# Performance work log

Measured on AMD Instinct MI355X. Metric: run time of the kernel, lower is better.

The kernel has to match this reference:

```python
import jax, jax.numpy as jnp
import numpy as np

NUM_EMBEDDINGS = 512
EMBEDDING_DIM = 128
COMMITMENT_COST = 0.6
MID_HR = 100.0
HR_RANGE = 70.0


def setup_inputs() -> dict:
    key = jax.random.key(0)
    k1, k2 = jax.random.split(key)
    inputs = jax.random.normal(k1, (64, 2048, EMBEDDING_DIM), dtype=jnp.float32)
    # torch init: uniform(-1/K, 1/K)
    emb_weight = jax.random.uniform(
        k2, (NUM_EMBEDDINGS, EMBEDDING_DIM), dtype=jnp.float32,
        minval=-1.0 / NUM_EMBEDDINGS, maxval=1.0 / NUM_EMBEDDINGS)
    scaling = jnp.ones((NUM_EMBEDDINGS,), dtype=jnp.float32)
    return {"inputs": inputs, "emb_weight": emb_weight, "scaling": scaling}


def reference(inputs, emb_weight, scaling):
    B, T, D = inputs.shape
    K = emb_weight.shape[0]
    flat = inputs.reshape(-1, D)  # [N, D]
    # squared L2 distances to all codes: [N, K]
    distances = (
        jnp.sum(flat * flat, axis=1, keepdims=True)
        + jnp.sum(emb_weight * emb_weight, axis=1)
        - 2.0 * flat @ emb_weight.T
    )
    hr_values = jnp.linspace(40.0, 180.0, K, dtype=jnp.float32)
    hr_weights = 1.0 + scaling * ((hr_values - MID_HR) / HR_RANGE)  # [K]
    encoding_indices = jnp.argmin(distances * hr_weights[None, :], axis=1)  # [N]
    # one-hot @ codebook == direct gather
    quantized = emb_weight[encoding_indices].reshape(inputs.shape)
    e_latent_loss = jnp.mean((jax.lax.stop_gradient(quantized) - inputs) ** 2)
    q_latent_loss = jnp.mean((quantized - jax.lax.stop_gradient(inputs)) ** 2)
    loss = q_latent_loss + COMMITMENT_COST * e_latent_loss
    # straight-through estimator
    quantized_st = inputs + jax.lax.stop_gradient(quantized - inputs)
    return quantized_st, loss, encoding_indices.reshape(B, T)
```

## Files before the change

kernel.cpp:

```cpp
#include <hip/hip_runtime.h>

#define NCODES 512
#define DIM 128
#define NROWS (64*2048)
#define QN (NROWS*DIM)
#define BLK_ROWS 512
#define NBLOCKS (NROWS/BLK_ROWS)
#define NWAVES 16

typedef __attribute__((ext_vector_type(8))) short short8;
typedef __attribute__((ext_vector_type(4))) float f32x4;

__device__ __forceinline__ unsigned short f2bf(float f) {
  unsigned u = __builtin_bit_cast(unsigned, f);
  u += 0x7FFFu + ((u >> 16) & 1u);
  return (unsigned short)(u >> 16);
}

#define GLOAD_LDS16(gp, lp) __builtin_amdgcn_global_load_lds( \
    (__attribute__((address_space(1))) void*)(gp), \
    (__attribute__((address_space(3))) void*)(lp), 16, 0, 0)

__global__ void vq_prep(const float* __restrict__ emb, const float* __restrict__ scaling,
                        unsigned short* __restrict__ emb_bf,
                        float* __restrict__ wv, float* __restrict__ wse,
                        float* __restrict__ wrcp) {
  int k = blockIdx.x;
  int l = threadIdx.x;
  float2 v = ((const float2*)(emb + k * DIM))[l];
  float ss = v.x * v.x + v.y * v.y;
#pragma unroll
  for (int m = 1; m < 64; m <<= 1) ss += __shfl_xor(ss, m);
  unsigned pack = (unsigned)f2bf(v.x) | ((unsigned)f2bf(v.y) << 16);
  ((unsigned*)emb_bf)[k * 64 + l] = pack;
  if (l == 0) {
    float hr = 40.0f + (float)k * (140.0f / 511.0f);
    float wt = 1.0f + scaling[k] * ((hr - 100.0f) * (1.0f / 70.0f));
    wv[k] = wt;
    wse[k] = wt * ss;
    wrcp[k] = 1.0f / wt;
  }
}

struct SmemT {
  unsigned short frag[NCODES * DIM];
  float w[NCODES];
  float wse[NCODES];
  float wrcp[NCODES];
  float lossp[NWAVES];
};

__global__ __launch_bounds__(1024, 4) void vq_main(
    const float* __restrict__ x,
    const float* __restrict__ emb32,
    const unsigned short* __restrict__ emb_bf,
    const float* __restrict__ wv,
    const float* __restrict__ wse,
    const float* __restrict__ wrcp,
    float* __restrict__ out_q,
    float* __restrict__ out_idx,
    float* __restrict__ out_loss) {
  __shared__ SmemT sm;
  const int tid = threadIdx.x;
  const int wave = tid >> 6, lane = tid & 63;
  const int g = lane >> 4, lr = lane & 15;
  const long rowbase = (long)blockIdx.x * BLK_ROWS + wave * 32;

  float4 xv[2][4][2];
#pragma unroll
  for (int rg = 0; rg < 2; rg++) {
    const float* xr = x + (rowbase + rg * 16 + lr) * DIM + g * 8;
#pragma unroll
    for (int c = 0; c < 4; c++) {
      xv[rg][c][0] = *(const float4*)(xr + c * 32);
      xv[rg][c][1] = *(const float4*)(xr + c * 32 + 4);
    }
  }

  {
    const uint4* src = (const uint4*)emb_bf;
#pragma unroll
    for (int i = 0; i < 8; i++) {
      int winst = wave * 8 + i;
      int d = winst * 64 + lane;
      int t = d >> 8, c = (d >> 6) & 3, gg = (d >> 4) & 3, rr = d & 15;
      int s = (t * 16 + rr) * 16 + c * 4 + gg;
      GLOAD_LDS16(src + s, (char*)sm.frag + winst * 1024);
    }
    if (tid < NCODES) {
      sm.w[tid] = wv[tid];
      sm.wse[tid] = wse[tid];
      sm.wrcp[tid] = wrcp[tid];
    }
  }

  short8 a[2][4];
  float sr[2][4];
  {
    float srow[2];
#pragma unroll
    for (int rg = 0; rg < 2; rg++) {
      float ss = 0.f;
#pragma unroll
      for (int c = 0; c < 4; c++) {
        float4 v0 = xv[rg][c][0];
        float4 v1 = xv[rg][c][1];
        ss += v0.x * v0.x + v0.y * v0.y + v0.z * v0.z + v0.w * v0.w;
        ss += v1.x * v1.x + v1.y * v1.y + v1.z * v1.z + v1.w * v1.w;
        short8 av;
        av[0] = (short)f2bf(v0.x); av[1] = (short)f2bf(v0.y);
        av[2] = (short)f2bf(v0.z); av[3] = (short)f2bf(v0.w);
        av[4] = (short)f2bf(v1.x); av[5] = (short)f2bf(v1.y);
        av[6] = (short)f2bf(v1.z); av[7] = (short)f2bf(v1.w);
        a[rg][c] = av;
      }
      ss += __shfl_xor(ss, 16);
      ss += __shfl_xor(ss, 32);
      srow[rg] = ss;
    }
#pragma unroll
    for (int rg = 0; rg < 2; rg++)
#pragma unroll
      for (int r = 0; r < 4; r++)
        sr[rg][r] = __shfl(srow[rg], g * 4 + r);
  }
  __syncthreads();

  unsigned pmin[2][4];
#pragma unroll
  for (int rg = 0; rg < 2; rg++)
#pragma unroll
    for (int r = 0; r < 4; r++) pmin[rg][r] = 0xFFFFFFFFu;

  const short8* __restrict__ bbase = (const short8*)sm.frag + lane;
#pragma unroll 2
  for (int t = 0; t < 32; t++) {
    const unsigned code = t * 16 + lr;
    const float wt = sm.w[code];
    const float bb = sm.wse[code];
    const float m2w = -2.0f * wt;
    f32x4 acc0 = {0.f, 0.f, 0.f, 0.f};
    f32x4 acc1 = {0.f, 0.f, 0.f, 0.f};
#pragma unroll
    for (int c = 0; c < 4; c++) {
      short8 bf = bbase[(t * 4 + c) * 64];
      acc0 = __builtin_amdgcn_mfma_f32_16x16x32_bf16(a[0][c], bf, acc0, 0, 0, 0);
      acc1 = __builtin_amdgcn_mfma_f32_16x16x32_bf16(a[1][c], bf, acc1, 0, 0, 0);
    }
#pragma unroll
    for (int r = 0; r < 4; r++) {
      float v0 = fmaf(m2w, acc0[r], fmaf(wt, sr[0][r], bb));
      float v1 = fmaf(m2w, acc1[r], fmaf(wt, sr[1][r], bb));
      unsigned u0 = (__builtin_bit_cast(unsigned, v0) & 0xFFFFFE00u) | code;
      unsigned u1 = (__builtin_bit_cast(unsigned, v1) & 0xFFFFFE00u) | code;
      pmin[0][r] = min(pmin[0][r], u0);
      pmin[1][r] = min(pmin[1][r], u1);
    }
  }

#pragma unroll
  for (int m = 1; m <= 8; m <<= 1) {
#pragma unroll
    for (int rg = 0; rg < 2; rg++)
#pragma unroll
      for (int r = 0; r < 4; r++) {
        unsigned o = (unsigned)__shfl_xor((int)pmin[rg][r], m);
        pmin[rg][r] = min(pmin[rg][r], o);
      }
  }

  const uint4* __restrict__ esrc = (const uint4*)emb32;
  uint4* __restrict__ outu = (uint4*)out_q + rowbase * 32;
  const int col = lane & 31;
  const int hi = lane >> 5;
  int scode[16];
#pragma unroll
  for (int it = 0; it < 16; it++) {
    const int row0 = 2 * it;
    const int rg = row0 >> 4;
    const int gn = (row0 >> 2) & 3;
    const int r0 = row0 & 3;
    int c0 = __shfl((int)pmin[rg][r0], gn * 16);
    int c1 = __shfl((int)pmin[rg][r0 + 1], gn * 16);
    scode[it] = (hi ? c1 : c0) & 511;
  }

  uint4 vbuf[8];
#pragma unroll
  for (int j = 0; j < 8; j++)
    vbuf[j] = esrc[scode[j] * 32 + col];

  {
    float l0 = 0.f;
#pragma unroll
    for (int rg = 0; rg < 2; rg++)
#pragma unroll
      for (int r = 0; r < 4; r++) {
        unsigned wn = pmin[rg][r];
        int ci = (int)(wn & 511u);
        float dist = __builtin_bit_cast(float, wn & 0xFFFFFE00u);
        l0 = fmaf(dist, sm.wrcp[ci], l0);
        if (lr == 0) out_idx[rowbase + rg * 16 + g * 4 + r] = (float)ci;
      }
    l0 += __shfl_xor(l0, 16);
    l0 += __shfl_xor(l0, 32);
    if (lane == 0) sm.lossp[wave] = l0;
  }

#pragma unroll
  for (int j = 0; j < 8; j++)
    outu[j * 64 + lane] = vbuf[j];
#pragma unroll
  for (int j = 0; j < 8; j++)
    vbuf[j] = esrc[scode[8 + j] * 32 + col];
#pragma unroll
  for (int j = 0; j < 8; j++)
    outu[(8 + j) * 64 + lane] = vbuf[j];

  __syncthreads();
  if (wave == 0 && lane < NWAVES) {
    float s = sm.lossp[lane];
#pragma unroll
    for (int m = 1; m < NWAVES; m <<= 1) s += __shfl_xor(s, m);
    if (lane == 0) atomicAdd(out_loss, s * (1.6f / (float)QN));
  }
}

extern "C" void kernel_launch(void* const* d_in, const int* in_sizes, int n_in,
                              void* d_out, int out_size, void* d_ws, size_t ws_size,
                              hipStream_t stream) {
  const float* x = (const float*)d_in[0];
  const float* emb = (const float*)d_in[1];
  const float* scaling = (const float*)d_in[2];

  float* out_q = (float*)d_out;
  float* out_loss = out_q + QN;
  float* out_idx = out_q + QN + 1;

  unsigned short* emb_bf = (unsigned short*)d_ws;
  float* wv = (float*)((char*)d_ws + NCODES * DIM * 2);
  float* wse = wv + NCODES;
  float* wrcp = wse + NCODES;

  hipMemsetAsync(out_loss, 0, sizeof(float), stream);
  vq_prep<<<NCODES, 64, 0, stream>>>(emb, scaling, emb_bf, wv, wse, wrcp);
  vq_main<<<NBLOCKS, 1024, 0, stream>>>(x, emb, emb_bf, wv, wse, wrcp,
                                        out_q, out_idx, out_loss);
}
```

Measured before the change: 49.27 us.

## Switch distance matmul from bf16 to fp8 MFMA with scaled codebook and smaller blocks

Converts inputs and codebook to fp8 (e4m3, codebook pre-scaled by 512 and laid out in fragment order during prep) and uses the 16x16x32 fp8 MFMA instead of bf16. This halves the shared-memory codebook footprint and the LDS read traffic. The block size is halved to 512 threads / 256 rows to raise occupancy. The risk is argmin mismatches from the much lower fp8 precision of both operands, especially near-tie distances, which could change the returned indices versus the reference.

```diff
diff --git a/kernel.cpp b/kernel.cpp
--- a/kernel.cpp
+++ b/kernel.cpp
@@ -4,25 +4,18 @@
 #define DIM 128
 #define NROWS (64*2048)
 #define QN (NROWS*DIM)
-#define BLK_ROWS 512
+#define BLK_ROWS 256
 #define NBLOCKS (NROWS/BLK_ROWS)
-#define NWAVES 16
-
-typedef __attribute__((ext_vector_type(8))) short short8;
+#define NWAVES 8
+
 typedef __attribute__((ext_vector_type(4))) float f32x4;
-
-__device__ __forceinline__ unsigned short f2bf(float f) {
-  unsigned u = __builtin_bit_cast(unsigned, f);
-  u += 0x7FFFu + ((u >> 16) & 1u);
-  return (unsigned short)(u >> 16);
-}
 
 #define GLOAD_LDS16(gp, lp) __builtin_amdgcn_global_load_lds( \
     (__attribute__((address_space(1))) void*)(gp), \
     (__attribute__((address_space(3))) void*)(lp), 16, 0, 0)
 
 __global__ void vq_prep(const float* __restrict__ emb, const float* __restrict__ scaling,
-                        unsigned short* __restrict__ emb_bf,
+                        unsigned char* __restrict__ e8frag,
                         float* __restrict__ wv, float* __restrict__ wse,
                         float* __restrict__ wrcp) {
   int k = blockIdx.x;
@@ -31,8 +24,11 @@
   float ss = v.x * v.x + v.y * v.y;
 #pragma unroll
   for (int m = 1; m < 64; m <<= 1) ss += __shfl_xor(ss, m);
-  unsigned pack = (unsigned)f2bf(v.x) | ((unsigned)f2bf(v.y) << 16);
-  ((unsigned*)emb_bf)[k * 64 + l] = pack;
+  int p = __builtin_amdgcn_cvt_pk_fp8_f32(v.x * 512.0f, v.y * 512.0f, 0, false);
+  int t = k >> 4, col = k & 15;
+  int c = l >> 4, g = (l >> 2) & 3, jp = l & 3;
+  *(unsigned short*)(e8frag + (((t * 4 + c) * 64 + g * 16 + col) << 3) + 2 * jp) =
+      (unsigned short)(p & 0xFFFF);
   if (l == 0) {
     float hr = 40.0f + (float)k * (140.0f / 511.0f);
     float wt = 1.0f + scaling[k] * ((hr - 100.0f) * (1.0f / 70.0f));
@@ -43,17 +39,17 @@
 }
 
 struct SmemT {
-  unsigned short frag[NCODES * DIM];
+  unsigned char frag[NCODES * DIM];
   float w[NCODES];
   float wse[NCODES];
   float wrcp[NCODES];
   float lossp[NWAVES];
 };
 
-__global__ __launch_bounds__(1024, 4) void vq_main(
+__global__ __launch_bounds__(512, 4) void vq_main(
     const float* __restrict__ x,
     const float* __restrict__ emb32,
-    const unsigned short* __restrict__ emb_bf,
+    const unsigned char* __restrict__ e8frag,
     const float* __restrict__ wv,
     const float* __restrict__ wse,
     const float* __restrict__ wrcp,
@@ -78,23 +74,16 @@
   }
 
   {
-    const uint4* src = (const uint4*)emb_bf;
 #pragma unroll
     for (int i = 0; i < 8; i++) {
-      int winst = wave * 8 + i;
-      int d = winst * 64 + lane;
-      int t = d >> 8, c = (d >> 6) & 3, gg = (d >> 4) & 3, rr = d & 15;
-      int s = (t * 16 + rr) * 16 + c * 4 + gg;
-      GLOAD_LDS16(src + s, (char*)sm.frag + winst * 1024);
-    }
-    if (tid < NCODES) {
-      sm.w[tid] = wv[tid];
-      sm.wse[tid] = wse[tid];
-      sm.wrcp[tid] = wrcp[tid];
-    }
-  }
-
-  short8 a[2][4];
+      int slot = i * 512 + tid;
+      GLOAD_LDS16(e8frag + slot * 16, sm.frag + slot * 16);
+    }
+    sm.w[tid] = wv[tid]; sm.wse[tid] = wse[tid]; sm.wrcp[tid] = wrcp[tid];
+    int t2 = tid + 512 - 512; (void)t2;
+  }
+
+  long a[2][4];
   float sr[2][4];
   {
     float srow[2];
@@ -107,12 +96,12 @@
         float4 v1 = xv[rg][c][1];
         ss += v0.x * v0.x + v0.y * v0.y + v0.z * v0.z + v0.w * v0.w;
         ss += v1.x * v1.x + v1.y * v1.y + v1.z * v1.z + v1.w * v1.w;
-        short8 av;
-        av[0] = (short)f2bf(v0.x); av[1] = (short)f2bf(v0.y);
-        av[2] = (short)f2bf(v0.z); av[3] = (short)f2bf(v0.w);
-        av[4] = (short)f2bf(v1.x); av[5] = (short)f2bf(v1.y);
-        av[6] = (short)f2bf(v1.z); av[7] = (short)f2bf(v1.w);
-        a[rg][c] = av;
+        int lo = __builtin_amdgcn_cvt_pk_fp8_f32(v0.x, v0.y, 0, false);
+        lo = __builtin_amdgcn_cvt_pk_fp8_f32(v0.z, v0.w, lo, true);
+        int hi = __builtin_amdgcn_cvt_pk_fp8_f32(v1.x, v1.y, 0, false);
+        hi = __builtin_amdgcn_cvt_pk_fp8_f32(v1.z, v1.w, hi, true);
+        a[rg][c] = (long)(((unsigned long long)(unsigned)hi << 32) |
+                          (unsigned long long)(unsigned)lo);
       }
       ss += __shfl_xor(ss, 16);
       ss += __shfl_xor(ss, 32);
@@ -132,20 +121,20 @@
 #pragma unroll
     for (int r = 0; r < 4; r++) pmin[rg][r] = 0xFFFFFFFFu;
 
-  const short8* __restrict__ bbase = (const short8*)sm.frag + lane;
+  const long* __restrict__ bbase = (const long*)sm.frag + lane;
 #pragma unroll 2
   for (int t = 0; t < 32; t++) {
     const unsigned code = t * 16 + lr;
     const float wt = sm.w[code];
     const float bb = sm.wse[code];
-    const float m2w = -2.0f * wt;
+    const float m2w = -2.0f * wt * (1.0f / 512.0f);
     f32x4 acc0 = {0.f, 0.f, 0.f, 0.f};
     f32x4 acc1 = {0.f, 0.f, 0.f, 0.f};
 #pragma unroll
     for (int c = 0; c < 4; c++) {
-      short8 bf = bbase[(t * 4 + c) * 64];
-      acc0 = __builtin_amdgcn_mfma_f32_16x16x32_bf16(a[0][c], bf, acc0, 0, 0, 0);
-      acc1 = __builtin_amdgcn_mfma_f32_16x16x32_bf16(a[1][c], bf, acc1, 0, 0, 0);
+      long bf = bbase[(t * 4 + c) * 64];
+      acc0 = __builtin_amdgcn_mfma_f32_16x16x32_fp8_fp8(a[0][c], bf, acc0, 0, 0, 0);
+      acc1 = __builtin_amdgcn_mfma_f32_16x16x32_fp8_fp8(a[1][c], bf, acc1, 0, 0, 0);
     }
 #pragma unroll
     for (int r = 0; r < 4; r++) {
@@ -172,7 +161,7 @@
   const uint4* __restrict__ esrc = (const uint4*)emb32;
   uint4* __restrict__ outu = (uint4*)out_q + rowbase * 32;
   const int col = lane & 31;
-  const int hi = lane >> 5;
+  const int hi2 = lane >> 5;
   int scode[16];
 #pragma unroll
   for (int it = 0; it < 16; it++) {
@@ -182,7 +171,7 @@
     const int r0 = row0 & 3;
     int c0 = __shfl((int)pmin[rg][r0], gn * 16);
     int c1 = __shfl((int)pmin[rg][r0 + 1], gn * 16);
-    scode[it] = (hi ? c1 : c0) & 511;
+    scode[it] = (hi2 ? c1 : c0) & 511;
   }
 
   uint4 vbuf[8];
@@ -237,13 +226,13 @@
   float* out_loss = out_q + QN;
   float* out_idx = out_q + QN + 1;
 
-  unsigned short* emb_bf = (unsigned short*)d_ws;
-  float* wv = (float*)((char*)d_ws + NCODES * DIM * 2);
+  unsigned char* e8frag = (unsigned char*)d_ws;
+  float* wv = (float*)((char*)d_ws + NCODES * DIM);
   float* wse = wv + NCODES;
   float* wrcp = wse + NCODES;
 
   hipMemsetAsync(out_loss, 0, sizeof(float), stream);
-  vq_prep<<<NCODES, 64, 0, stream>>>(emb, scaling, emb_bf, wv, wse, wrcp);
-  vq_main<<<NBLOCKS, 1024, 0, stream>>>(x, emb, emb_bf, wv, wse, wrcp,
-                                        out_q, out_idx, out_loss);
+  vq_prep<<<NCODES, 64, 0, stream>>>(emb, scaling, e8frag, wv, wse, wrcp);
+  vq_main<<<NBLOCKS, 512, 0, stream>>>(x, emb, e8frag, wv, wse, wrcp,
+                                       out_q, out_idx, out_loss);
 }
```

Result: faster. 43.02 us (-12.7%).
